# Kernel tuning notes

Hardware: AMD Instinct MI355X
Metric: run time of the kernel (lower is better)

The kernel has to match this reference:

```python
import jax, jax.numpy as jnp
import numpy as np

N_NODES = 100000


def _gcn_layer(x, W, b, src, dst, dinv):
    # x: [N, din]; W: [din, dout]; src/dst: [E+N] (self-loops included); dinv: [N]
    h = x @ W                                   # [N, dout] small GEMM
    norm = dinv[src] * dinv[dst]                # [E+N]
    msg = h[src] * norm[:, None]                # [E+N, dout] gather
    out = jax.ops.segment_sum(msg, dst, num_segments=N_NODES)  # scatter-add
    return jax.nn.relu(out + b)


def setup_inputs() -> dict:
    key = jax.random.key(0)
    ks = jax.random.split(key, 8)
    d_in, d_h = 128, 128
    x = jax.random.normal(ks[0], (N_NODES, d_in), dtype=jnp.float32)
    edge_index = jax.random.randint(ks[1], (2, 1600000), 0, N_NODES, dtype=jnp.int64)
    def glorot(k, din, dout):
        lim = np.sqrt(6.0 / (din + dout)).astype(np.float32)
        return jax.random.uniform(k, (din, dout), jnp.float32, -lim, lim)
    W1 = glorot(ks[2], d_in, d_h); b1 = jnp.zeros((d_h,), jnp.float32)
    W2 = glorot(ks[3], d_h, d_h); b2 = jnp.zeros((d_h,), jnp.float32)
    W3 = glorot(ks[4], d_h, d_h); b3 = jnp.zeros((d_h,), jnp.float32)
    return {"x": x, "W1": W1, "b1": b1, "W2": W2, "b2": b2,
            "W3": W3, "b3": b3, "edge_index": edge_index}


def reference(x, W1, b1, W2, b2, W3, b3, edge_index):
    # GCNConv (Kipf & Welling): D^{-1/2}(A+I)D^{-1/2} X W + b, per layer, with ReLU.
    loop = jnp.arange(N_NODES, dtype=edge_index.dtype)
    src = jnp.concatenate([edge_index[0], loop])  # self-loops appended
    dst = jnp.concatenate([edge_index[1], loop])
    deg = jax.ops.segment_sum(jnp.ones_like(dst, dtype=x.dtype), dst,
                              num_segments=N_NODES)
    dinv = jnp.where(deg > 0, jax.lax.rsqrt(deg), 0.0)
    h = _gcn_layer(x, W1, b1, src, dst, dinv)
    h = _gcn_layer(h, W2, b2, src, dst, dinv)
    h = _gcn_layer(h, W3, b3, src, dst, dinv)
    return h
```

## Files before the change

### kernel.cpp

```cpp
#include <hip/hip_runtime.h>
#include <hip/hip_fp16.h>
#include <math.h>

#define NN 100000
#define DD 128
#define SCAN_CHUNK 2048

typedef short short8 __attribute__((ext_vector_type(8)));
typedef float f32x4 __attribute__((ext_vector_type(4)));

__global__ __launch_bounds__(256) void hist_rank_kernel(const int* __restrict__ dst, int E,
                                                        int* __restrict__ deg,
                                                        int* __restrict__ rank) {
    int i = blockIdx.x * 256 + threadIdx.x;
    int e = i * 4;
    if (e + 3 < E) {
        int4 d4 = ((const int4*)dst)[i];
        int4 r4;
        r4.x = atomicAdd(&deg[d4.x], 1);
        r4.y = atomicAdd(&deg[d4.y], 1);
        r4.z = atomicAdd(&deg[d4.z], 1);
        r4.w = atomicAdd(&deg[d4.w], 1);
        ((int4*)rank)[i] = r4;
    } else {
        for (; e < E; ++e) rank[e] = atomicAdd(&deg[dst[e]], 1);
    }
}

__global__ __launch_bounds__(256) void scan1_kernel(const int* __restrict__ deg,
                                                    int* __restrict__ chunkSum,
                                                    float* __restrict__ dinv, int n) {
    __shared__ int lds[256];
    int tid = threadIdx.x;
    int base = blockIdx.x * SCAN_CHUNK + tid * 8;
    int s = 0;
    #pragma unroll
    for (int j = 0; j < 8; ++j) {
        int idx = base + j;
        if (idx < n) {
            int d = deg[idx];
            s += d;
            dinv[idx] = rsqrtf((float)d + 1.0f);
        }
    }
    lds[tid] = s;
    __syncthreads();
    for (int d = 128; d > 0; d >>= 1) {
        if (tid < d) lds[tid] += lds[tid + d];
        __syncthreads();
    }
    if (tid == 0) chunkSum[blockIdx.x] = lds[0];
}

__global__ void scan2_kernel(int* __restrict__ chunkSum, int* __restrict__ chunkOff,
                             int nb, int* __restrict__ offsets) {
    __shared__ int lds[512];
    int tid = threadIdx.x;
    if (tid < nb) lds[tid] = chunkSum[tid];
    __syncthreads();
    if (tid == 0) {
        int run = 0;
        for (int i = 0; i < nb; ++i) {
            int v = lds[i];
            lds[i] = run;
            run += v;
        }
        offsets[NN] = run;
    }
    __syncthreads();
    if (tid < nb) chunkOff[tid] = lds[tid];
}

__global__ __launch_bounds__(256) void scan3_kernel(const int* __restrict__ deg,
                                                    const int* __restrict__ chunkOff,
                                                    int* __restrict__ offsets, int n) {
    __shared__ int lds[256];
    int tid = threadIdx.x;
    int base = blockIdx.x * SCAN_CHUNK + tid * 8;
    int v[8];
    int tsum = 0;
    #pragma unroll
    for (int j = 0; j < 8; ++j) {
        int idx = base + j;
        v[j] = (idx < n) ? deg[idx] : 0;
        tsum += v[j];
    }
    lds[tid] = tsum;
    __syncthreads();
    for (int d = 1; d < 256; d <<= 1) {
        int t = (tid >= d) ? lds[tid - d] : 0;
        __syncthreads();
        lds[tid] += t;
        __syncthreads();
    }
    int excl = lds[tid] - tsum;
    int off0 = chunkOff[blockIdx.x] + excl;
    int run = 0;
    #pragma unroll
    for (int j = 0; j < 8; ++j) {
        int idx = base + j;
        if (idx < n) offsets[idx] = off0 + run;
        run += v[j];
    }
}

__global__ __launch_bounds__(256) void fill_kernel(const int* __restrict__ src,
                                                   const int* __restrict__ dst,
                                                   const int* __restrict__ rank, int E,
                                                   const int* __restrict__ offsets,
                                                   int* __restrict__ csr) {
    int i = blockIdx.x * 256 + threadIdx.x;
    int e = i * 4;
    if (e + 3 < E) {
        int4 d4 = ((const int4*)dst)[i];
        int4 s4 = ((const int4*)src)[i];
        int4 r4 = ((const int4*)rank)[i];
        int o0 = offsets[d4.x];
        int o1 = offsets[d4.y];
        int o2 = offsets[d4.z];
        int o3 = offsets[d4.w];
        csr[o0 + r4.x] = s4.x;
        csr[o1 + r4.y] = s4.y;
        csr[o2 + r4.z] = s4.z;
        csr[o3 + r4.w] = s4.w;
    } else {
        for (; e < E; ++e) csr[offsets[dst[e]] + rank[e]] = src[e];
    }
}

__device__ __forceinline__ unsigned short f2bf(float f) {
    unsigned int u = __float_as_uint(f);
    unsigned int r = u + 0x7FFFu + ((u >> 16) & 1u);
    return (unsigned short)(r >> 16);
}

__device__ __forceinline__ void split8(const float* v, short8& hi, short8& lo) {
    #pragma unroll
    for (int j = 0; j < 8; ++j) {
        float f = v[j];
        unsigned short h = f2bf(f);
        float fl = f - __uint_as_float(((unsigned int)h) << 16);
        hi[j] = (short)h;
        lo[j] = (short)f2bf(fl);
    }
}

__global__ __launch_bounds__(256, 2) void gemm_norm_kernel(
    const float* __restrict__ X, const float* __restrict__ W,
    const float* __restrict__ dinv, __half* __restrict__ G)
{
    __shared__ uint4 whf[2048];
    __shared__ uint4 wlf[2048];

    const int tid  = threadIdx.x;
    const int base = blockIdx.x * 128;
    const int lane = tid & 63;
    const int wv   = tid >> 6;
    const int kg   = lane >> 4;
    const int mcol = lane & 15;

    #pragma unroll
    for (int p = 0; p < 8; ++p) {
        int i = tid + p * 256;
        int lane_e = i & 63;
        int ks = (i >> 6) & 3;
        int cf = i >> 8;
        int colb = cf * 16 + (lane_e & 15);
        int rowb = ks * 32 + (lane_e >> 4) * 8;
        float wvv[8];
        #pragma unroll
        for (int j = 0; j < 8; ++j) wvv[j] = W[(rowb + j) * DD + colb];
        short8 h, l;
        split8(wvv, h, l);
        union { short8 s; uint4 u; } ch, cl;
        ch.s = h; cl.s = l;
        whf[i] = ch.u;
        wlf[i] = cl.u;
    }

    short8 ah[2][4], al[2][4];
    #pragma unroll
    for (int rf = 0; rf < 2; ++rf) {
        int arow = base + wv * 32 + rf * 16 + mcol;
        if (arow >= NN) arow = NN - 1;
        const float* xr = X + (size_t)arow * DD;
        #pragma unroll
        for (int ks = 0; ks < 4; ++ks) {
            int k0 = ks * 32 + kg * 8;
            float av[8];
            *(float4*)&av[0] = *(const float4*)&xr[k0];
            *(float4*)&av[4] = *(const float4*)&xr[k0 + 4];
            split8(av, ah[rf][ks], al[rf][ks]);
        }
    }
    __syncthreads();

    #pragma unroll 1
    for (int cf = 0; cf < 8; ++cf) {
        f32x4 acc0 = {0.f, 0.f, 0.f, 0.f};
        f32x4 acc1 = {0.f, 0.f, 0.f, 0.f};
        #pragma unroll
        for (int ks = 0; ks < 4; ++ks) {
            union { uint4 u; short8 s; } bh, bl;
            bh.u = whf[(cf * 4 + ks) * 64 + lane];
            bl.u = wlf[(cf * 4 + ks) * 64 + lane];
            acc0 = __builtin_amdgcn_mfma_f32_16x16x32_bf16(ah[0][ks], bh.s, acc0, 0, 0, 0);
            acc0 = __builtin_amdgcn_mfma_f32_16x16x32_bf16(al[0][ks], bh.s, acc0, 0, 0, 0);
            acc0 = __builtin_amdgcn_mfma_f32_16x16x32_bf16(ah[0][ks], bl.s, acc0, 0, 0, 0);
            acc1 = __builtin_amdgcn_mfma_f32_16x16x32_bf16(ah[1][ks], bh.s, acc1, 0, 0, 0);
            acc1 = __builtin_amdgcn_mfma_f32_16x16x32_bf16(al[1][ks], bh.s, acc1, 0, 0, 0);
            acc1 = __builtin_amdgcn_mfma_f32_16x16x32_bf16(ah[1][ks], bl.s, acc1, 0, 0, 0);
        }
        #pragma unroll
        for (int rf = 0; rf < 2; ++rf) {
            const f32x4 acc = rf ? acc1 : acc0;
            int row0 = base + wv * 32 + rf * 16 + kg * 4;
            if (row0 < NN) {
                float dv[4];
                *(float4*)dv = *(const float4*)&dinv[row0];
                #pragma unroll
                for (int j = 0; j < 4; ++j) {
                    G[(size_t)(row0 + j) * DD + cf * 16 + mcol] =
                        __float2half(acc[j] * dv[j]);
                }
            }
        }
    }
}

__global__ __launch_bounds__(256) void agg_kernel(
    const __half* __restrict__ g, const float* __restrict__ dinv,
    const int* __restrict__ off, const int* __restrict__ csr,
    const float* __restrict__ bias, float* __restrict__ out)
{
    int node = (blockIdx.x * 256 + threadIdx.x) >> 6;
    if (node >= NN) return;
    int lane = threadIdx.x & 63;
    const __half2* __restrict__ g2 = (const __half2*)g;

    float2 acc0 = __half22float2(g2[node * 64 + lane]);
    float2 acc1 = make_float2(0.f, 0.f);

    int e = off[node], end = off[node + 1];
    int cnt = end - e;
    int e8end = e + (cnt & ~7);

    if (e < e8end) {
        int idx[8];
        #pragma unroll
        for (int j = 0; j < 8; ++j) idx[j] = csr[e + j];
        e += 8;
        for (; e < e8end; e += 8) {
            int nidx[8];
            #pragma unroll
            for (int j = 0; j < 8; ++j) nidx[j] = csr[e + j];
            #pragma unroll
            for (int j = 0; j < 8; j += 2) {
                float2 v0 = __half22float2(g2[idx[j] * 64 + lane]);
                float2 v1 = __half22float2(g2[idx[j + 1] * 64 + lane]);
                acc0.x += v0.x; acc0.y += v0.y;
                acc1.x += v1.x; acc1.y += v1.y;
            }
            #pragma unroll
            for (int j = 0; j < 8; ++j) idx[j] = nidx[j];
        }
        #pragma unroll
        for (int j = 0; j < 8; j += 2) {
            float2 v0 = __half22float2(g2[idx[j] * 64 + lane]);
            float2 v1 = __half22float2(g2[idx[j + 1] * 64 + lane]);
            acc0.x += v0.x; acc0.y += v0.y;
            acc1.x += v1.x; acc1.y += v1.y;
        }
    }
    for (; e < end; ++e) {
        float2 v = __half22float2(g2[csr[e] * 64 + lane]);
        acc0.x += v.x; acc0.y += v.y;
    }

    float di = dinv[node];
    float2 bb = ((const float2*)bias)[lane];
    float2 o;
    o.x = fmaxf(fmaf(acc0.x + acc1.x, di, bb.x), 0.f);
    o.y = fmaxf(fmaf(acc0.y + acc1.y, di, bb.y), 0.f);
    ((float2*)out)[node * 64 + lane] = o;
}

extern "C" void kernel_launch(void* const* d_in, const int* in_sizes, int n_in,
                              void* d_out, int out_size, void* d_ws, size_t ws_size,
                              hipStream_t stream)
{
    const float* x  = (const float*)d_in[0];
    const float* W1 = (const float*)d_in[1];
    const float* b1 = (const float*)d_in[2];
    const float* W2 = (const float*)d_in[3];
    const float* b2 = (const float*)d_in[4];
    const float* W3 = (const float*)d_in[5];
    const float* b3 = (const float*)d_in[6];
    const int*   ei = (const int*)d_in[7];

    const int E = in_sizes[7] / 2;
    const int* src = ei;
    const int* dst = ei + E;

    float* out = (float*)d_out;

    char* wsb = (char*)d_ws;
    size_t p = 0;
    int* deg      = (int*)(wsb + p); p += ((size_t)NN * 4 + 1023) & ~1023ull;
    int* offsets  = (int*)(wsb + p); p += ((size_t)(NN + 1) * 4 + 1023) & ~1023ull;
    int* chunkSum = (int*)(wsb + p); p += 4096;
    int* chunkOff = (int*)(wsb + p); p += 4096;
    int* csr      = (int*)(wsb + p); p += ((size_t)E * 4 + 1023) & ~1023ull;
    int* rank     = (int*)(wsb + p); p += ((size_t)E * 4 + 1023) & ~1023ull;
    float* dinv   = (float*)(wsb + p); p += ((size_t)NN * 4 + 1023) & ~1023ull;
    __half* g     = (__half*)(wsb + p); p += (size_t)NN * DD * 2;

    const int NB = (NN + SCAN_CHUNK - 1) / SCAN_CHUNK;

    hipMemsetAsync(deg, 0, (size_t)NN * 4, stream);
    hist_rank_kernel<<<(E / 4 + 256) / 256 + 1, 256, 0, stream>>>(dst, E, deg, rank);
    scan1_kernel<<<NB, 256, 0, stream>>>(deg, chunkSum, dinv, NN);
    scan2_kernel<<<1, 512, 0, stream>>>(chunkSum, chunkOff, NB, offsets);
    scan3_kernel<<<NB, 256, 0, stream>>>(deg, chunkOff, offsets, NN);
    fill_kernel<<<(E / 4 + 256) / 256 + 1, 256, 0, stream>>>(src, dst, rank, E, offsets, csr);

    const int gemm_grid = (NN + 127) / 128;
    const int agg_grid  = ((size_t)NN * 64 + 255) / 256;

    gemm_norm_kernel<<<gemm_grid, 256, 0, stream>>>(x, W1, dinv, g);
    agg_kernel<<<agg_grid, 256, 0, stream>>>(g, dinv, offsets, csr, b1, out);
    gemm_norm_kernel<<<gemm_grid, 256, 0, stream>>>(out, W2, dinv, g);
    agg_kernel<<<agg_grid, 256, 0, stream>>>(g, dinv, offsets, csr, b2, out);
    gemm_norm_kernel<<<gemm_grid, 256, 0, stream>>>(out, W3, dinv, g);
    agg_kernel<<<agg_grid, 256, 0, stream>>>(g, dinv, offsets, csr, b3, out);
}
```

Measured before the change: 413.0 us.

## Store intermediate activations in fp16, presplit weights once, use persistent agg grid

Intermediate layer activations are now written and read as fp16 instead of fp32, which halves that traffic between the aggregation and GEMM kernels. The bf16 hi/lo split of all three weight matrices moves into a single small kernel, so each GEMM block copies the presplit weights instead of recomputing them. The aggregation kernel becomes a grid-stride persistent loop over groups of four nodes with a fixed block count. The fp16 activations add rounding error in the intermediate layers.

```diff
diff --git a/kernel.cpp b/kernel.cpp
--- a/kernel.cpp
+++ b/kernel.cpp
@@ -5,6 +5,7 @@
 #define NN 100000
 #define DD 128
 #define SCAN_CHUNK 2048
+#define AGG_BLOCKS 2048
 
 typedef short short8 __attribute__((ext_vector_type(8)));
 typedef float f32x4 __attribute__((ext_vector_type(4)));
@@ -145,8 +146,35 @@
     }
 }
 
+__global__ __launch_bounds__(256) void wsplit3_kernel(const float* __restrict__ W1,
+                                                      const float* __restrict__ W2,
+                                                      const float* __restrict__ W3,
+                                                      uint4* __restrict__ wh,
+                                                      uint4* __restrict__ wl) {
+    int b = blockIdx.x;
+    int layer = b >> 3;
+    const float* W = (layer == 0) ? W1 : (layer == 1) ? W2 : W3;
+    int i = (b & 7) * 256 + threadIdx.x;
+    int lane_e = i & 63;
+    int ks = (i >> 6) & 3;
+    int cf = i >> 8;
+    int colb = cf * 16 + (lane_e & 15);
+    int rowb = ks * 32 + (lane_e >> 4) * 8;
+    float wvv[8];
+    #pragma unroll
+    for (int j = 0; j < 8; ++j) wvv[j] = W[(rowb + j) * DD + colb];
+    short8 h, l;
+    split8(wvv, h, l);
+    union { short8 s; uint4 u; } ch, cl;
+    ch.s = h; cl.s = l;
+    wh[layer * 2048 + i] = ch.u;
+    wl[layer * 2048 + i] = cl.u;
+}
+
+template <typename InT>
 __global__ __launch_bounds__(256, 2) void gemm_norm_kernel(
-    const float* __restrict__ X, const float* __restrict__ W,
+    const InT* __restrict__ X, const uint4* __restrict__ whg,
+    const uint4* __restrict__ wlg,
     const float* __restrict__ dinv, __half* __restrict__ G)
 {
     __shared__ uint4 whf[2048];
@@ -162,20 +190,8 @@
     #pragma unroll
     for (int p = 0; p < 8; ++p) {
         int i = tid + p * 256;
-        int lane_e = i & 63;
-        int ks = (i >> 6) & 3;
-        int cf = i >> 8;
-        int colb = cf * 16 + (lane_e & 15);
-        int rowb = ks * 32 + (lane_e >> 4) * 8;
-        float wvv[8];
-        #pragma unroll
-        for (int j = 0; j < 8; ++j) wvv[j] = W[(rowb + j) * DD + colb];
-        short8 h, l;
-        split8(wvv, h, l);
-        union { short8 s; uint4 u; } ch, cl;
-        ch.s = h; cl.s = l;
-        whf[i] = ch.u;
-        wlf[i] = cl.u;
+        whf[i] = whg[i];
+        wlf[i] = wlg[i];
     }
 
     short8 ah[2][4], al[2][4];
@@ -183,13 +199,20 @@
     for (int rf = 0; rf < 2; ++rf) {
         int arow = base + wv * 32 + rf * 16 + mcol;
         if (arow >= NN) arow = NN - 1;
-        const float* xr = X + (size_t)arow * DD;
+        const InT* xr = X + (size_t)arow * DD;
         #pragma unroll
         for (int ks = 0; ks < 4; ++ks) {
             int k0 = ks * 32 + kg * 8;
             float av[8];
-            *(float4*)&av[0] = *(const float4*)&xr[k0];
-            *(float4*)&av[4] = *(const float4*)&xr[k0 + 4];
+            if constexpr (sizeof(InT) == 4) {
+                *(float4*)&av[0] = *(const float4*)&xr[k0];
+                *(float4*)&av[4] = *(const float4*)&xr[k0 + 4];
+            } else {
+                union { uint4 u; __half h[8]; } hv;
+                hv.u = *(const uint4*)&xr[k0];
+                #pragma unroll
+                for (int j = 0; j < 8; ++j) av[j] = __half2float(hv.h[j]);
+            }
             split8(av, ah[rf][ks], al[rf][ks]);
         }
     }
@@ -228,32 +251,48 @@
     }
 }
 
+template <typename OutT>
 __global__ __launch_bounds__(256) void agg_kernel(
     const __half* __restrict__ g, const float* __restrict__ dinv,
     const int* __restrict__ off, const int* __restrict__ csr,
-    const float* __restrict__ bias, float* __restrict__ out)
+    const float* __restrict__ bias, OutT* __restrict__ out)
 {
-    int node = (blockIdx.x * 256 + threadIdx.x) >> 6;
-    if (node >= NN) return;
-    int lane = threadIdx.x & 63;
+    const int wid  = threadIdx.x >> 6;
+    const int lane = threadIdx.x & 63;
     const __half2* __restrict__ g2 = (const __half2*)g;
-
-    float2 acc0 = __half22float2(g2[node * 64 + lane]);
-    float2 acc1 = make_float2(0.f, 0.f);
-
-    int e = off[node], end = off[node + 1];
-    int cnt = end - e;
-    int e8end = e + (cnt & ~7);
-
-    if (e < e8end) {
-        int idx[8];
-        #pragma unroll
-        for (int j = 0; j < 8; ++j) idx[j] = csr[e + j];
-        e += 8;
-        for (; e < e8end; e += 8) {
-            int nidx[8];
+    const float2 bb = ((const float2*)bias)[lane];
+    const int ngroups = (NN + 3) / 4;
+
+    for (int grp = blockIdx.x; grp < ngroups; grp += AGG_BLOCKS) {
+        int node = grp * 4 + wid;
+        if (node >= NN) continue;
+
+        float2 acc0 = __half22float2(g2[node * 64 + lane]);
+        float2 acc1 = make_float2(0.f, 0.f);
+
+        int e = off[node], end = off[node + 1];
+        int cnt = end - e;
+        int e8end = e + (cnt & ~7);
+
+        if (e < e8end) {
+            int idx[8];
             #pragma unroll
-            for (int j = 0; j < 8; ++j) nidx[j] = csr[e + j];
+            for (int j = 0; j < 8; ++j) idx[j] = csr[e + j];
+            e += 8;
+            for (; e < e8end; e += 8) {
+                int nidx[8];
+                #pragma unroll
+                for (int j = 0; j < 8; ++j) nidx[j] = csr[e + j];
+                #pragma unroll
+                for (int j = 0; j < 8; j += 2) {
+                    float2 v0 = __half22float2(g2[idx[j] * 64 + lane]);
+                    float2 v1 = __half22float2(g2[idx[j + 1] * 64 + lane]);
+                    acc0.x += v0.x; acc0.y += v0.y;
+                    acc1.x += v1.x; acc1.y += v1.y;
+                }
+                #pragma unroll
+                for (int j = 0; j < 8; ++j) idx[j] = nidx[j];
+            }
             #pragma unroll
             for (int j = 0; j < 8; j += 2) {
                 float2 v0 = __half22float2(g2[idx[j] * 64 + lane]);
@@ -261,28 +300,21 @@
                 acc0.x += v0.x; acc0.y += v0.y;
                 acc1.x += v1.x; acc1.y += v1.y;
             }
-            #pragma unroll
-            for (int j = 0; j < 8; ++j) idx[j] = nidx[j];
-        }
-        #pragma unroll
-        for (int j = 0; j < 8; j += 2) {
-            float2 v0 = __half22float2(g2[idx[j] * 64 + lane]);
-            float2 v1 = __half22float2(g2[idx[j + 1] * 64 + lane]);
-            acc0.x += v0.x; acc0.y += v0.y;
-            acc1.x += v1.x; acc1.y += v1.y;
-        }
-    }
-    for (; e < end; ++e) {
-        float2 v = __half22float2(g2[csr[e] * 64 + lane]);
-        acc0.x += v.x; acc0.y += v.y;
-    }
-
-    float di = dinv[node];
-    float2 bb = ((const float2*)bias)[lane];
-    float2 o;
-    o.x = fmaxf(fmaf(acc0.x + acc1.x, di, bb.x), 0.f);
-    o.y = fmaxf(fmaf(acc0.y + acc1.y, di, bb.y), 0.f);
-    ((float2*)out)[node * 64 + lane] = o;
+        }
+        for (; e < end; ++e) {
+            float2 v = __half22float2(g2[csr[e] * 64 + lane]);
+            acc0.x += v.x; acc0.y += v.y;
+        }
+
+        float di = dinv[node];
+        float ox = fmaxf(fmaf(acc0.x + acc1.x, di, bb.x), 0.f);
+        float oy = fmaxf(fmaf(acc0.y + acc1.y, di, bb.y), 0.f);
+        if constexpr (sizeof(OutT) == 4) {
+            ((float2*)out)[node * 64 + lane] = make_float2(ox, oy);
+        } else {
+            ((__half2*)out)[node * 64 + lane] = __floats2half2_rn(ox, oy);
+        }
+    }
 }
 
 extern "C" void kernel_launch(void* const* d_in, const int* in_sizes, int n_in,
@@ -313,7 +345,10 @@
     int* csr      = (int*)(wsb + p); p += ((size_t)E * 4 + 1023) & ~1023ull;
     int* rank     = (int*)(wsb + p); p += ((size_t)E * 4 + 1023) & ~1023ull;
     float* dinv   = (float*)(wsb + p); p += ((size_t)NN * 4 + 1023) & ~1023ull;
+    uint4* wh     = (uint4*)(wsb + p); p += 3 * 2048 * sizeof(uint4);
+    uint4* wl     = (uint4*)(wsb + p); p += 3 * 2048 * sizeof(uint4);
     __half* g     = (__half*)(wsb + p); p += (size_t)NN * DD * 2;
+    __half* h_act = (__half*)(wsb + p); p += (size_t)NN * DD * 2;
 
     const int NB = (NN + SCAN_CHUNK - 1) / SCAN_CHUNK;
 
@@ -323,14 +358,14 @@
     scan2_kernel<<<1, 512, 0, stream>>>(chunkSum, chunkOff, NB, offsets);
     scan3_kernel<<<NB, 256, 0, stream>>>(deg, chunkOff, offsets, NN);
     fill_kernel<<<(E / 4 + 256) / 256 + 1, 256, 0, stream>>>(src, dst, rank, E, offsets, csr);
+    wsplit3_kernel<<<24, 256, 0, stream>>>(W1, W2, W3, wh, wl);
 
     const int gemm_grid = (NN + 127) / 128;
-    const int agg_grid  = ((size_t)NN * 64 + 255) / 256;
-
-    gemm_norm_kernel<<<gemm_grid, 256, 0, stream>>>(x, W1, dinv, g);
-    agg_kernel<<<agg_grid, 256, 0, stream>>>(g, dinv, offsets, csr, b1, out);
-    gemm_norm_kernel<<<gemm_grid, 256, 0, stream>>>(out, W2, dinv, g);
-    agg_kernel<<<agg_grid, 256, 0, stream>>>(g, dinv, offsets, csr, b2, out);
-    gemm_norm_kernel<<<gemm_grid, 256, 0, stream>>>(out, W3, dinv, g);
-    agg_kernel<<<agg_grid, 256, 0, stream>>>(g, dinv, offsets, csr, b3, out);
-}
+
+    gemm_norm_kernel<float><<<gemm_grid, 256, 0, stream>>>(x, wh, wl, dinv, g);
+    agg_kernel<__half><<<AGG_BLOCKS, 256, 0, stream>>>(g, dinv, offsets, csr, b1, h_act);
+    gemm_norm_kernel<__half><<<gemm_grid, 256, 0, stream>>>(h_act, wh + 2048, wl + 2048, dinv, g);
+    agg_kernel<__half><<<AGG_BLOCKS, 256, 0, stream>>>(g, dinv, offsets, csr, b2, h_act);
+    gemm_norm_kernel<__half><<<gemm_grid, 256, 0, stream>>>(h_act, wh + 4096, wl + 4096, dinv, g);
+    agg_kernel<float><<<AGG_BLOCKS, 256, 0, stream>>>(g, dinv, offsets, csr, b3, out);
+}
```

New measurement: 404.8 us. 1.02x faster.
